# Kernel tuning notes

Measured on AMD Instinct MI355X. Metric: run time of the kernel, lower is better.

The kernel has to match this reference:

```python
import jax, jax.numpy as jnp
import numpy as np

B, S, D, H = 4, 2048, 1024, 16
HD = D // H  # head size = 64

def setup_inputs() -> dict:
    key = jax.random.key(0)
    ks = jax.random.split(key, 9)
    s = 1.0 / np.sqrt(D)
    inp = {"x": jax.random.normal(ks[0], (B, S, D), dtype=jnp.float32)}
    for i, n in enumerate(["q", "k", "v", "o"]):
        inp[f"W{n}"] = jax.random.uniform(ks[1 + 2 * i], (D, D), minval=-s, maxval=s, dtype=jnp.float32)
        inp[f"b{n}"] = jax.random.uniform(ks[2 + 2 * i], (D,), minval=-s, maxval=s, dtype=jnp.float32)
    return inp

def reference(x, Wq, bq, Wk, bk, Wv, bv, Wo, bo):
    b, s, d = x.shape
    # project and split heads: [b, h, s, hd]
    def heads(y):
        return y.reshape(b, s, H, HD).transpose(0, 2, 1, 3)
    q = heads(x @ Wq.T + bq)
    k = heads(x @ Wk.T + bk)
    v = heads(x @ Wv.T + bv)
    scores = jnp.einsum('bhqd,bhkd->bhqk', q, k) / jnp.sqrt(jnp.float32(HD))
    attn = jax.nn.softmax(scores, axis=-1)
    ctx = jnp.einsum('bhqk,bhkd->bhqd', attn, v)
    ctx = ctx.transpose(0, 2, 1, 3).reshape(b, s, d)
    return ctx @ Wo.T + bo
```

## Files before the change

kernel.cpp:

```cpp
#include <hip/hip_runtime.h>
#include <hip/hip_bf16.h>

typedef __bf16 bf16;
typedef __bf16 bf16x8 __attribute__((ext_vector_type(8)));
typedef __bf16 bf16x4 __attribute__((ext_vector_type(4)));
typedef float f32x4 __attribute__((ext_vector_type(4)));
typedef float f32x16 __attribute__((ext_vector_type(16)));
typedef unsigned int u32;
typedef u32 u32x4 __attribute__((ext_vector_type(4)));

#define B_ 4
#define S_ 2048
#define D_ 1024
#define H_ 16
#define HD_ 64
#define LOG2E 1.4426950408889634f

static __device__ __forceinline__ f32x4 mfma16(bf16x8 a, bf16x8 b, f32x4 c) {
  return __builtin_amdgcn_mfma_f32_16x16x32_bf16(a, b, c, 0, 0, 0);
}
static __device__ __forceinline__ f32x16 mfma32(bf16x8 a, bf16x8 b, f32x16 c) {
  return __builtin_amdgcn_mfma_f32_32x32x16_bf16(a, b, c, 0, 0, 0);
}
static __device__ __forceinline__ void gload_lds16(const void* g, void* l) {
  __builtin_amdgcn_global_load_lds(
      (const __attribute__((address_space(1))) void*)g,
      (__attribute__((address_space(3))) void*)l, 16, 0, 0);
}
static __device__ __forceinline__ u32 pack2(float lo, float hi) {
  union { bf16 h[2]; u32 u; } un;
  un.h[0] = (bf16)lo; un.h[1] = (bf16)hi;
  return un.u;
}

__global__ void cvt_kernel(const float* __restrict__ in, bf16* __restrict__ out, int n4) {
  int i = blockIdx.x * blockDim.x + threadIdx.x;
  const int stride = gridDim.x * blockDim.x;
  for (; i < n4; i += stride) {
    float4 v = reinterpret_cast<const float4*>(in)[i];
    bf16x4 o;
    o[0] = (bf16)v.x; o[1] = (bf16)v.y; o[2] = (bf16)v.z; o[3] = (bf16)v.w;
    reinterpret_cast<bf16x4*>(out)[i] = o;
  }
}
__global__ void cvtw_kernel(const float* __restrict__ w0, const float* __restrict__ w1,
                            const float* __restrict__ w2, const float* __restrict__ w3,
                            bf16* __restrict__ o0, bf16* __restrict__ o1,
                            bf16* __restrict__ o2, bf16* __restrict__ o3, int n4) {
  const float* in = blockIdx.y == 0 ? w0 : blockIdx.y == 1 ? w1 : blockIdx.y == 2 ? w2 : w3;
  bf16* out = blockIdx.y == 0 ? o0 : blockIdx.y == 1 ? o1 : blockIdx.y == 2 ? o2 : o3;
  const int i = blockIdx.x * blockDim.x + threadIdx.x;
  float4 v = reinterpret_cast<const float4*>(in)[i];
  bf16x4 o;
  o[0] = (bf16)v.x; o[1] = (bf16)v.y; o[2] = (bf16)v.z; o[3] = (bf16)v.w;
  reinterpret_cast<bf16x4*>(out)[i] = o;
}

template<bool OUT_BF16, bool BIAS_ROW>
__global__ __launch_bounds__(512, 2)
void gemm2(const bf16* __restrict__ A, const bf16* __restrict__ W,
           const float* __restrict__ bias, void* __restrict__ Cout,
           int M, int N, int K, float scale) {
  __shared__ __align__(16) char lds[147456];
  const int tid = threadIdx.x;
  const int wave = tid >> 6;
  const int lane = tid & 63;
  const int g = lane >> 4, r16 = lane & 15;
  const int m0 = blockIdx.y * 256, n0 = blockIdx.x * 128;
  const int wm = (wave >> 1) * 64, wn = (wave & 1) * 64;

  f32x4 acc[4][4] = {};

  const int srow = tid >> 3;
  const int scol = ((tid & 7) ^ (srow & 7)) * 8;
  const int wdst = wave * 1024;
  const int nkt = K >> 6;

  auto stage = [&](int bi, int t) {
    char* buf = lds + bi * 49152;
    const int kb = t << 6;
#pragma unroll
    for (int q = 0; q < 4; ++q)
      gload_lds16(&A[(size_t)(m0 + q * 64 + srow) * K + kb + scol],
                  buf + q * 8192 + wdst);
#pragma unroll
    for (int q = 0; q < 2; ++q)
      gload_lds16(&W[(size_t)(n0 + q * 64 + srow) * K + kb + scol],
                  buf + 32768 + q * 8192 + wdst);
  };

  stage(0, 0);
  stage(1, 1);
  int cur = 0;

  for (int t = 0; t < nkt; ++t) {
    if (t + 1 < nkt) asm volatile("s_waitcnt vmcnt(6)" ::: "memory");
    else             asm volatile("s_waitcnt vmcnt(0)" ::: "memory");
    __builtin_amdgcn_s_barrier();
    int nx2 = cur + 2; if (nx2 >= 3) nx2 -= 3;
    if (t + 2 < nkt) stage(nx2, t + 2);

    const char* bufA = lds + cur * 49152;
    const char* bufB = bufA + 32768;
#pragma unroll
    for (int kk = 0; kk < 2; ++kk) {
      bf16x8 af[4], bfr[4];
#pragma unroll
      for (int i = 0; i < 4; ++i) {
        const int ra = wm + i * 16 + r16;
        af[i]  = *reinterpret_cast<const bf16x8*>(
            bufA + ra * 128 + (((4 * kk + g) ^ (ra & 7)) * 16));
        const int rb = wn + i * 16 + r16;
        bfr[i] = *reinterpret_cast<const bf16x8*>(
            bufB + rb * 128 + (((4 * kk + g) ^ (rb & 7)) * 16));
      }
      __builtin_amdgcn_s_setprio(1);
#pragma unroll
      for (int i = 0; i < 4; ++i)
#pragma unroll
        for (int j = 0; j < 4; ++j)
          acc[i][j] = mfma16(af[i], bfr[j], acc[i][j]);
      __builtin_amdgcn_s_setprio(0);
    }
    cur = (cur + 1 == 3) ? 0 : cur + 1;
  }

#pragma unroll
  for (int i = 0; i < 4; ++i) {
#pragma unroll
    for (int j = 0; j < 4; ++j) {
      const int col = n0 + wn + j * 16 + r16;
      float bcol = BIAS_ROW ? 0.f : bias[col];
#pragma unroll
      for (int r = 0; r < 4; ++r) {
        const int row = m0 + wm + i * 16 + g * 4 + r;
        const float bv = BIAS_ROW ? bias[row] : bcol;
        const float v = (acc[i][j][r] + bv) * scale;
        if (OUT_BF16)
          reinterpret_cast<bf16*>(Cout)[(size_t)row * N + col] = (bf16)v;
        else
          reinterpret_cast<float*>(Cout)[(size_t)row * N + col] = v;
      }
    }
  }
}

__global__ __launch_bounds__(256)
void attn_kernel(const bf16* __restrict__ Q, const bf16* __restrict__ K,
                 const bf16* __restrict__ Vt, bf16* __restrict__ CTX) {
  const unsigned nwg = gridDim.x * gridDim.y;
  const unsigned lid = blockIdx.x + gridDim.x * blockIdx.y;
  const unsigned swzid = (lid & 7) * (nwg >> 3) + (lid >> 3);
  const int bh = (int)(swzid >> 4);
  const int q0 = (int)(swzid & 15) * 128;
  const int h = bh & (H_ - 1), b = bh >> 4;
  const int tid = threadIdx.x, wave = tid >> 6, lane = tid & 63;
  const int l32 = lane & 31, hi = lane >> 5;

  const bf16* Qb  = Q  + ((size_t)b * S_) * D_ + h * HD_;
  const bf16* Kb  = K  + ((size_t)b * S_) * D_ + h * HD_;
  const bf16* Vtb = Vt + (size_t)(h * HD_) * (B_ * S_) + b * S_;

  __shared__ __align__(16) char lds[32768];
  char* kb0 = lds;
  char* kb1 = lds + 8192;
  char* vb0 = lds + 16384;
  char* vb1 = lds + 24576;

  const int q = q0 + wave * 32 + l32;
  bf16x8 qf[4];
#pragma unroll
  for (int ks = 0; ks < 4; ++ks)
    qf[ks] = *reinterpret_cast<const bf16x8*>(&Qb[(size_t)q * D_ + ks * 16 + hi * 8]);

  f32x16 ctx0 = {}, ctx1 = {};
  float lrun = 0.f;

  const int krow0 = wave * 16 + (lane >> 3);
  const int xs = ((lane & 7) ^ (lane >> 3)) * 8;
  const int stoff = wave * 2048;
  const int swl = (l32 & 7) << 4;

  auto stage = [&](char* kd, char* vd, int kv0) {
    const size_t kg = (size_t)(kv0 + krow0) * D_ + xs;
    const size_t vg = (size_t)krow0 * (B_ * S_) + kv0 + xs;
    gload_lds16(Kb + kg,                   kd + stoff);
    gload_lds16(Kb + kg + 8 * D_,          kd + stoff + 1024);
    gload_lds16(Vtb + vg,                  vd + stoff);
    gload_lds16(Vtb + vg + 8 * (B_ * S_),  vd + stoff + 1024);
  };

  auto qkt = [&](f32x16& s0, f32x16& s1, const char* bK) {
    const f32x16 z = {};
    __builtin_amdgcn_s_setprio(1);
    {
      const int co = (hi * 16) ^ swl;
      bf16x8 kf0 = *reinterpret_cast<const bf16x8*>(bK + l32 * 128 + co);
      bf16x8 kf1 = *reinterpret_cast<const bf16x8*>(bK + (32 + l32) * 128 + co);
      s0 = mfma32(kf0, qf[0], z);
      s1 = mfma32(kf1, qf[0], z);
    }
#pragma unroll
    for (int ks = 1; ks < 4; ++ks) {
      const int co = (ks * 32 + hi * 16) ^ swl;
      bf16x8 kf0 = *reinterpret_cast<const bf16x8*>(bK + l32 * 128 + co);
      bf16x8 kf1 = *reinterpret_cast<const bf16x8*>(bK + (32 + l32) * 128 + co);
      s0 = mfma32(kf0, qf[ks], s0);
      s1 = mfma32(kf1, qf[ks], s1);
    }
    __builtin_amdgcn_s_setprio(0);
  };

  auto smpv = [&](const f32x16& s0, const f32x16& s1, const char* bV) {
    u32 w0[8], w1[8];
    float r0 = 0.f, r1 = 0.f;
#pragma unroll
    for (int a = 0; a < 4; ++a)
#pragma unroll
      for (int c = 0; c < 2; ++c) {
        const float e0 = __builtin_amdgcn_exp2f(s0[4 * a + 2 * c]);
        const float e1 = __builtin_amdgcn_exp2f(s0[4 * a + 2 * c + 1]);
        w0[2 * a + c] = pack2(e0, e1); r0 += e0 + e1;
        const float f0 = __builtin_amdgcn_exp2f(s1[4 * a + 2 * c]);
        const float f1 = __builtin_amdgcn_exp2f(s1[4 * a + 2 * c + 1]);
        w1[2 * a + c] = pack2(f0, f1); r1 += f0 + f1;
      }
    float rs = r0 + r1;
    rs += __shfl_xor(rs, 32);
    lrun += rs;
#pragma unroll
    for (int T = 0; T < 2; ++T) {
      const u32* w = T ? w1 : w0;
#pragma unroll
      for (int k1 = 0; k1 < 2; ++k1) {
        auto rA = __builtin_amdgcn_permlane32_swap((int)w[4 * k1 + 0], (int)w[4 * k1 + 2], false, false);
        auto rB = __builtin_amdgcn_permlane32_swap((int)w[4 * k1 + 1], (int)w[4 * k1 + 3], false, false);
        u32x4 fw;
        fw[0] = (u32)rA[0]; fw[1] = (u32)rB[0]; fw[2] = (u32)rA[1]; fw[3] = (u32)rB[1];
        const bf16x8 pa = __builtin_bit_cast(bf16x8, fw);
        const int ksp = T * 2 + k1;
        const int co = (ksp * 32 + hi * 16) ^ swl;
        bf16x8 vf0 = *reinterpret_cast<const bf16x8*>(bV + l32 * 128 + co);
        bf16x8 vf1 = *reinterpret_cast<const bf16x8*>(bV + (32 + l32) * 128 + co);
        __builtin_amdgcn_s_setprio(1);
        ctx0 = mfma32(pa, vf0, ctx0);
        ctx1 = mfma32(pa, vf1, ctx1);
        __builtin_amdgcn_s_setprio(0);
      }
    }
  };

  stage(kb0, vb0, 0);
  __syncthreads();

  for (int t = 0; t < 32; ++t) {
    const char* kc = (t & 1) ? kb1 : kb0;
    const char* vc = (t & 1) ? vb1 : vb0;
    if (t < 31) stage((t & 1) ? kb0 : kb1, (t & 1) ? vb0 : vb1, (t + 1) * 64);
    f32x16 s0, s1;
    qkt(s0, s1, kc);
    smpv(s0, s1, vc);
    __syncthreads();
  }

  char* Cw = lds + wave * 4096;
#pragma unroll
  for (int rg = 0; rg < 16; ++rg) {
    const int ql = (rg & 3) + 8 * (rg >> 2) + 4 * hi;
    const float inv = 1.0f / __shfl(lrun, ql);
    const int swq = (ql & 7) << 4;
    *reinterpret_cast<bf16*>(Cw + ql * 128 + ((l32 * 2) ^ swq)) = (bf16)(ctx0[rg] * inv);
    *reinterpret_cast<bf16*>(Cw + ql * 128 + ((64 + l32 * 2) ^ swq)) = (bf16)(ctx1[rg] * inv);
  }
  asm volatile("" ::: "memory");
#pragma unroll
  for (int i = 0; i < 4; ++i) {
    const int s = i * 64 + lane;
    const int row = s >> 3, cs = (s & 7) * 16;
    bf16x8 v = *reinterpret_cast<const bf16x8*>(Cw + row * 128 + (cs ^ ((row & 7) << 4)));
    *reinterpret_cast<bf16x8*>(
        &CTX[(size_t)(b * S_ + q0 + wave * 32 + row) * D_ + h * HD_ + cs / 2]) = v;
  }
}

extern "C" void kernel_launch(void* const* d_in, const int* in_sizes, int n_in,
                              void* d_out, int out_size, void* d_ws, size_t ws_size,
                              hipStream_t stream) {
  const float* x  = (const float*)d_in[0];
  const float* Wq = (const float*)d_in[1]; const float* bq = (const float*)d_in[2];
  const float* Wk = (const float*)d_in[3]; const float* bk = (const float*)d_in[4];
  const float* Wv = (const float*)d_in[5]; const float* bv = (const float*)d_in[6];
  const float* Wo = (const float*)d_in[7]; const float* bo = (const float*)d_in[8];

  char* ws = (char*)d_ws;
  const size_t MB = 1048576;
  bf16* xb  = (bf16*)(ws);
  bf16* wqb = (bf16*)(ws + 16 * MB);
  bf16* wkb = (bf16*)(ws + 18 * MB);
  bf16* wvb = (bf16*)(ws + 20 * MB);
  bf16* wob = (bf16*)(ws + 22 * MB);
  bf16* qb  = (bf16*)(ws + 24 * MB);
  bf16* kb  = (bf16*)(ws + 40 * MB);
  bf16* vtb = (bf16*)(ws + 56 * MB);
  bf16* ctx = (bf16*)(ws + 72 * MB);

  cvt_kernel<<<2048, 256, 0, stream>>>(x, xb, 2097152);
  cvtw_kernel<<<dim3(1024, 4), 256, 0, stream>>>(Wq, Wk, Wv, Wo, wqb, wkb, wvb, wob, 262144);

  dim3 gq(1024 / 128, 8192 / 256);
  gemm2<true,  false><<<gq, 512, 0, stream>>>(xb, wqb, bq, qb, 8192, 1024, 1024, 0.125f * LOG2E);
  gemm2<true,  false><<<gq, 512, 0, stream>>>(xb, wkb, bk, kb, 8192, 1024, 1024, 1.0f);
  dim3 gv(8192 / 128, 1024 / 256);
  gemm2<true,  true ><<<gv, 512, 0, stream>>>(wvb, xb, bv, vtb, 1024, 8192, 1024, 1.0f);

  attn_kernel<<<dim3(2048 / 128, B_ * H_), 256, 0, stream>>>(qb, kb, vtb, ctx);

  gemm2<false, false><<<gq, 512, 0, stream>>>(ctx, wob, bo, d_out, 8192, 1024, 1024, 1.0f);
}
```

Baseline: 214.1 us.

## Compute softmax row sums via MFMA with ones and unroll double-buffer loop

Replaces the VALU accumulation of exp sums plus the cross-lane shuffle with an extra MFMA that multiplies the probability fragment by a ones vector, so row sums land in an accumulator already laid out like ctx. The main loop is manually unrolled by two so buffer pointers are compile-time constants, and the swizzled LDS offsets and staging pointers are precomputed or incremented instead of recomputed each iteration. This cuts VALU work and shuffles but adds 50% more MFMAs in the PV stage and 16 extra accumulator registers. Row sums now come from bf16-rounded probabilities, which matches what the PV product uses.

```diff
diff --git a/kernel.cpp b/kernel.cpp
--- a/kernel.cpp
+++ b/kernel.cpp
@@ -162,10 +162,10 @@
   const bf16* Vtb = Vt + (size_t)(h * HD_) * (B_ * S_) + b * S_;
 
   __shared__ __align__(16) char lds[32768];
-  char* kb0 = lds;
-  char* kb1 = lds + 8192;
-  char* vb0 = lds + 16384;
-  char* vb1 = lds + 24576;
+  char* const kb0 = lds;
+  char* const kb1 = lds + 8192;
+  char* const vb0 = lds + 16384;
+  char* const vb1 = lds + 24576;
 
   const int q = q0 + wave * 32 + l32;
   bf16x8 qf[4];
@@ -173,76 +173,77 @@
   for (int ks = 0; ks < 4; ++ks)
     qf[ks] = *reinterpret_cast<const bf16x8*>(&Qb[(size_t)q * D_ + ks * 16 + hi * 8]);
 
+  bf16x8 onesf;
+#pragma unroll
+  for (int j = 0; j < 8; ++j) onesf[j] = (bf16)1.0f;
+
   f32x16 ctx0 = {}, ctx1 = {};
-  float lrun = 0.f;
+  f32x16 lacc = {};
 
   const int krow0 = wave * 16 + (lane >> 3);
   const int xs = ((lane & 7) ^ (lane >> 3)) * 8;
   const int stoff = wave * 2048;
   const int swl = (l32 & 7) << 4;
-
-  auto stage = [&](char* kd, char* vd, int kv0) {
-    const size_t kg = (size_t)(kv0 + krow0) * D_ + xs;
-    const size_t vg = (size_t)krow0 * (B_ * S_) + kv0 + xs;
-    gload_lds16(Kb + kg,                   kd + stoff);
-    gload_lds16(Kb + kg + 8 * D_,          kd + stoff + 1024);
-    gload_lds16(Vtb + vg,                  vd + stoff);
-    gload_lds16(Vtb + vg + 8 * (B_ * S_),  vd + stoff + 1024);
+  int coa[4];
+#pragma unroll
+  for (int ks = 0; ks < 4; ++ks) coa[ks] = (ks * 32 + hi * 16) ^ swl;
+  const int rA = l32 * 128, rB = (32 + l32) * 128;
+
+  const bf16* Kst = Kb  + (size_t)krow0 * D_ + xs;
+  const bf16* Vst = Vtb + (size_t)krow0 * (B_ * S_) + xs;
+
+  auto stage = [&](char* kd, char* vd) {
+    gload_lds16(Kst,                  kd + stoff);
+    gload_lds16(Kst + 8 * D_,         kd + stoff + 1024);
+    gload_lds16(Vst,                  vd + stoff);
+    gload_lds16(Vst + 8 * (B_ * S_),  vd + stoff + 1024);
+    Kst += 64 * D_;
+    Vst += 64;
   };
 
-  auto qkt = [&](f32x16& s0, f32x16& s1, const char* bK) {
+  auto compute = [&](const char* bK, const char* bV) {
+    f32x16 s0, s1;
     const f32x16 z = {};
     __builtin_amdgcn_s_setprio(1);
     {
-      const int co = (hi * 16) ^ swl;
-      bf16x8 kf0 = *reinterpret_cast<const bf16x8*>(bK + l32 * 128 + co);
-      bf16x8 kf1 = *reinterpret_cast<const bf16x8*>(bK + (32 + l32) * 128 + co);
+      bf16x8 kf0 = *reinterpret_cast<const bf16x8*>(bK + rA + coa[0]);
+      bf16x8 kf1 = *reinterpret_cast<const bf16x8*>(bK + rB + coa[0]);
       s0 = mfma32(kf0, qf[0], z);
       s1 = mfma32(kf1, qf[0], z);
     }
 #pragma unroll
     for (int ks = 1; ks < 4; ++ks) {
-      const int co = (ks * 32 + hi * 16) ^ swl;
-      bf16x8 kf0 = *reinterpret_cast<const bf16x8*>(bK + l32 * 128 + co);
-      bf16x8 kf1 = *reinterpret_cast<const bf16x8*>(bK + (32 + l32) * 128 + co);
+      bf16x8 kf0 = *reinterpret_cast<const bf16x8*>(bK + rA + coa[ks]);
+      bf16x8 kf1 = *reinterpret_cast<const bf16x8*>(bK + rB + coa[ks]);
       s0 = mfma32(kf0, qf[ks], s0);
       s1 = mfma32(kf1, qf[ks], s1);
     }
     __builtin_amdgcn_s_setprio(0);
-  };
-
-  auto smpv = [&](const f32x16& s0, const f32x16& s1, const char* bV) {
     u32 w0[8], w1[8];
-    float r0 = 0.f, r1 = 0.f;
 #pragma unroll
     for (int a = 0; a < 4; ++a)
 #pragma unroll
       for (int c = 0; c < 2; ++c) {
-        const float e0 = __builtin_amdgcn_exp2f(s0[4 * a + 2 * c]);
-        const float e1 = __builtin_amdgcn_exp2f(s0[4 * a + 2 * c + 1]);
-        w0[2 * a + c] = pack2(e0, e1); r0 += e0 + e1;
-        const float f0 = __builtin_amdgcn_exp2f(s1[4 * a + 2 * c]);
-        const float f1 = __builtin_amdgcn_exp2f(s1[4 * a + 2 * c + 1]);
-        w1[2 * a + c] = pack2(f0, f1); r1 += f0 + f1;
+        w0[2 * a + c] = pack2(__builtin_amdgcn_exp2f(s0[4 * a + 2 * c]),
+                              __builtin_amdgcn_exp2f(s0[4 * a + 2 * c + 1]));
+        w1[2 * a + c] = pack2(__builtin_amdgcn_exp2f(s1[4 * a + 2 * c]),
+                              __builtin_amdgcn_exp2f(s1[4 * a + 2 * c + 1]));
       }
-    float rs = r0 + r1;
-    rs += __shfl_xor(rs, 32);
-    lrun += rs;
 #pragma unroll
     for (int T = 0; T < 2; ++T) {
       const u32* w = T ? w1 : w0;
 #pragma unroll
       for (int k1 = 0; k1 < 2; ++k1) {
-        auto rA = __builtin_amdgcn_permlane32_swap((int)w[4 * k1 + 0], (int)w[4 * k1 + 2], false, false);
-        auto rB = __builtin_amdgcn_permlane32_swap((int)w[4 * k1 + 1], (int)w[4 * k1 + 3], false, false);
+        auto rAp = __builtin_amdgcn_permlane32_swap((int)w[4 * k1 + 0], (int)w[4 * k1 + 2], false, false);
+        auto rBp = __builtin_amdgcn_permlane32_swap((int)w[4 * k1 + 1], (int)w[4 * k1 + 3], false, false);
         u32x4 fw;
-        fw[0] = (u32)rA[0]; fw[1] = (u32)rB[0]; fw[2] = (u32)rA[1]; fw[3] = (u32)rB[1];
+        fw[0] = (u32)rAp[0]; fw[1] = (u32)rBp[0]; fw[2] = (u32)rAp[1]; fw[3] = (u32)rBp[1];
         const bf16x8 pa = __builtin_bit_cast(bf16x8, fw);
-        const int ksp = T * 2 + k1;
-        const int co = (ksp * 32 + hi * 16) ^ swl;
-        bf16x8 vf0 = *reinterpret_cast<const bf16x8*>(bV + l32 * 128 + co);
-        bf16x8 vf1 = *reinterpret_cast<const bf16x8*>(bV + (32 + l32) * 128 + co);
+        const int co = coa[T * 2 + k1];
+        bf16x8 vf0 = *reinterpret_cast<const bf16x8*>(bV + rA + co);
+        bf16x8 vf1 = *reinterpret_cast<const bf16x8*>(bV + rB + co);
         __builtin_amdgcn_s_setprio(1);
+        lacc = mfma32(pa, onesf, lacc);
         ctx0 = mfma32(pa, vf0, ctx0);
         ctx1 = mfma32(pa, vf1, ctx1);
         __builtin_amdgcn_s_setprio(0);
@@ -250,24 +251,27 @@
     }
   };
 
-  stage(kb0, vb0, 0);
+  stage(kb0, vb0);
   __syncthreads();
-
-  for (int t = 0; t < 32; ++t) {
-    const char* kc = (t & 1) ? kb1 : kb0;
-    const char* vc = (t & 1) ? vb1 : vb0;
-    if (t < 31) stage((t & 1) ? kb0 : kb1, (t & 1) ? vb0 : vb1, (t + 1) * 64);
-    f32x16 s0, s1;
-    qkt(s0, s1, kc);
-    smpv(s0, s1, vc);
+  for (int tt = 0; tt < 15; ++tt) {
+    stage(kb1, vb1);
+    compute(kb0, vb0);
     __syncthreads();
-  }
+    stage(kb0, vb0);
+    compute(kb1, vb1);
+    __syncthreads();
+  }
+  stage(kb1, vb1);
+  compute(kb0, vb0);
+  __syncthreads();
+  compute(kb1, vb1);
+  __syncthreads();
 
   char* Cw = lds + wave * 4096;
 #pragma unroll
   for (int rg = 0; rg < 16; ++rg) {
     const int ql = (rg & 3) + 8 * (rg >> 2) + 4 * hi;
-    const float inv = 1.0f / __shfl(lrun, ql);
+    const float inv = 1.0f / lacc[rg];
     const int swq = (ql & 7) << 4;
     *reinterpret_cast<bf16*>(Cw + ql * 128 + ((l32 * 2) ^ swq)) = (bf16)(ctx0[rg] * inv);
     *reinterpret_cast<bf16*>(Cw + ql * 128 + ((64 + l32 * 2) ^ swq)) = (bf16)(ctx1[rg] * inv);
```

Result: faster. 203.1 us (-5.1%).
